# Performance work log

Measured on AMD Instinct MI355X. Metric: run time of the kernel, lower is better.

## Reference

```python
import jax, jax.numpy as jnp
import numpy as np

D = 256   # input_dim (also per-head dim)
H = 8     # num_heads
B = 32
S = 1024


def setup_inputs() -> dict:
    key = jax.random.key(0)
    ks = jax.random.split(key, 9)
    scale = 1.0 / np.sqrt(D)
    x = jax.random.normal(ks[0], (B, S, D), dtype=jnp.float32)
    Wk = jax.random.normal(ks[1], (D, D * H), dtype=jnp.float32) * scale
    bk = jnp.zeros((D * H,), dtype=jnp.float32)
    Wv = jax.random.normal(ks[2], (D, D * H), dtype=jnp.float32) * scale
    bv = jnp.zeros((D * H,), dtype=jnp.float32)
    query = jax.random.normal(ks[3], (H, D), dtype=jnp.float32)
    Wo = jax.random.normal(ks[4], (D * H, D), dtype=jnp.float32) / np.sqrt(D * H)
    bo = jnp.zeros((D,), dtype=jnp.float32)
    return {"x": x, "Wk": Wk, "bk": bk, "Wv": Wv, "bv": bv,
            "query": query, "Wo": Wo, "bo": bo}


def reference(x, Wk, bk, Wv, bv, query, Wo, bo):
    b, s, _ = x.shape
    # keys/values: [B, S, H, D]
    keys = (x @ Wk + bk).reshape(b, s, H, D)
    values = (x @ Wv + bv).reshape(b, s, H, D)
    # per-head single-query scores over sequence: [B, S, H]
    scores = jnp.einsum("bshd,hd->bsh", keys, query)
    attn = jax.nn.softmax(scores, axis=1)
    # attention-pooled values per head: [B, H, D] -> concat [B, H*D]
    pooled = jnp.einsum("bsh,bshd->bhd", attn, values).reshape(b, H * D)
    return pooled @ Wo + bo
```

## Files before the change

### kernel.cpp

```cpp
#include <hip/hip_runtime.h>

#define D 256
#define H 8
#define B 32
#define S 1024
#define SCH 16
#define SCS 64

#define OFF_QK     0
#define OFF_SB     2048
#define OFF_ML     2056
#define OFF_XWP    10248
#define OFF_POOLED 1058824

__global__ void __launch_bounds__(256) k_prep(
        const float* __restrict__ Wk, const float* __restrict__ bk,
        const float* __restrict__ query, const float* __restrict__ bo,
        const float* __restrict__ bv,
        float* __restrict__ qk, float* __restrict__ sb,
        float* __restrict__ out, float* __restrict__ pooled) {
    __shared__ float red[256];
    const int h  = blockIdx.x >> 5;
    const int kc = blockIdx.x & 31;
    const int t  = threadIdx.x;
    const int kl = t >> 5;
    const int dq = t & 31;
    const int k  = kc * 8 + kl;
    const int d0 = dq * 8;
    const float* wrow = Wk + (size_t)k * (D * H) + h * D + d0;
    const float* qrow = query + h * D + d0;
    const float4 w0 = *(const float4*)(wrow);
    const float4 w1 = *(const float4*)(wrow + 4);
    const float4 q0 = *(const float4*)(qrow);
    const float4 q1 = *(const float4*)(qrow + 4);
    float acc = w0.x * q0.x + w0.y * q0.y + w0.z * q0.z + w0.w * q0.w
              + w1.x * q1.x + w1.y * q1.y + w1.z * q1.z + w1.w * q1.w;
    #pragma unroll
    for (int msk = 1; msk < 32; msk <<= 1) acc += __shfl_xor(acc, msk);
    if (dq == 0) qk[h * D + k] = acc;
    if (kc == 0) {
        red[t] = bk[h * D + t] * query[h * D + t];
        __syncthreads();
        for (int st = 128; st > 0; st >>= 1) {
            if (t < st) red[t] += red[t + st];
            __syncthreads();
        }
        if (t == 0) sb[h] = red[0];
    }
    pooled[(size_t)kc * (D * H) + h * D + t] = bv[h * D + t];
    if (h == 0) out[(size_t)kc * D + t] = bo[t];
}

__global__ void __launch_bounds__(256) k_fused(
        const float* __restrict__ x, const float* __restrict__ qk,
        const float* __restrict__ sb, float* __restrict__ xwp,
        float2* __restrict__ mlbuf) {
    const int b  = blockIdx.x >> 4;
    const int c  = blockIdx.x & 15;
    const int s0 = c * SCS;
    const int t  = threadIdx.x;
    __shared__ float qkL[H * D];
    __shared__ float sbL[H];
    __shared__ float sc[SCS][H];
    {
        float4* q4 = (float4*)qkL;
        q4[t]       = ((const float4*)qk)[t];
        q4[t + 256] = ((const float4*)qk)[t + 256];
        if (t < H) sbL[t] = sb[t];
    }
    __syncthreads();

    {
        const int sl = t >> 2;
        const int dq = t & 3;
        const int d0 = dq * 64;
        const float* xrow = x + ((size_t)(b * S + s0 + sl)) * D + d0;
        float accA[H] = {};
        #pragma unroll
        for (int j0 = 0; j0 < 16; j0++) {
            const int j = (j0 + dq * 4) & 15;
            const float4 xv = *(const float4*)(xrow + j * 4);
            #pragma unroll
            for (int hh = 0; hh < H; hh++) {
                const float4 qv = *(const float4*)(&qkL[hh * D + d0 + j * 4]);
                accA[hh] += xv.x * qv.x + xv.y * qv.y + xv.z * qv.z + xv.w * qv.w;
            }
        }
        #pragma unroll
        for (int hh = 0; hh < H; hh++) {
            accA[hh] += __shfl_xor(accA[hh], 1);
            accA[hh] += __shfl_xor(accA[hh], 2);
        }
        if (dq == 0) {
            #pragma unroll
            for (int hh = 0; hh < H; hh++)
                sc[sl][hh] = accA[hh] + sbL[hh];
        }
    }
    __syncthreads();

    {
        const int hh = t >> 5;
        const int u  = t & 31;
        const float v0 = sc[u][hh], v1 = sc[u + 32][hh];
        float m = fmaxf(v0, v1);
        #pragma unroll
        for (int msk = 1; msk < 32; msk <<= 1) m = fmaxf(m, __shfl_xor(m, msk));
        const float e0 = __expf(v0 - m), e1 = __expf(v1 - m);
        float sum = e0 + e1;
        #pragma unroll
        for (int msk = 1; msk < 32; msk <<= 1) sum += __shfl_xor(sum, msk);
        sc[u][hh] = e0;
        sc[u + 32][hh] = e1;
        if (u == 0) mlbuf[((size_t)(b * SCH + c)) * H + hh] = make_float2(m, sum);
    }
    __syncthreads();

    {
        float acc2[H] = {};
        const float* xp = x + ((size_t)(b * S + s0)) * D + t;
        #pragma unroll 4
        for (int s = 0; s < SCS; s++) {
            const float xv = xp[(size_t)s * D];
            const float4 pa = *(const float4*)(&sc[s][0]);
            const float4 pb = *(const float4*)(&sc[s][4]);
            acc2[0] += pa.x * xv; acc2[1] += pa.y * xv;
            acc2[2] += pa.z * xv; acc2[3] += pa.w * xv;
            acc2[4] += pb.x * xv; acc2[5] += pb.y * xv;
            acc2[6] += pb.z * xv; acc2[7] += pb.w * xv;
        }
        #pragma unroll
        for (int hh = 0; hh < H; hh++)
            xwp[(((size_t)(b * SCH + c)) * H + hh) * D + t] = acc2[hh];
    }
}

__global__ void __launch_bounds__(256) k_pooled(
        const float* __restrict__ xwp, const float2* __restrict__ mlbuf,
        const float* __restrict__ Wv, float* __restrict__ pooled) {
    const int blk = blockIdx.x;
    const int bh  = blk >> 1;
    const int dh  = blk & 1;
    const int b = bh >> 3, h = bh & 7;
    const int j = threadIdx.x;
    __shared__ float xwL[D / 2];
    __shared__ float scaleL[SCH];
    __shared__ float2 mlL[SCH];
    if (j < SCH) mlL[j] = mlbuf[((size_t)(b * SCH + j)) * H + h];
    __syncthreads();
    if (j == 0) {
        float M = -1e30f;
        for (int cc = 0; cc < SCH; cc++) M = fmaxf(M, mlL[cc].x);
        float L = 0.f;
        for (int cc = 0; cc < SCH; cc++) L += mlL[cc].y * __expf(mlL[cc].x - M);
        const float invL = 1.f / L;
        for (int cc = 0; cc < SCH; cc++) scaleL[cc] = __expf(mlL[cc].x - M) * invL;
    }
    __syncthreads();
    if (j < D / 2) {
        const int d = dh * (D / 2) + j;
        float acc = 0.f;
        #pragma unroll
        for (int cc = 0; cc < SCH; cc++)
            acc += xwp[(((size_t)(b * SCH + cc)) * H + h) * D + d] * scaleL[cc];
        xwL[j] = acc;
    }
    __syncthreads();
    const float* wcol = Wv + (size_t)(dh * (D / 2)) * (D * H) + h * D + j;
    float a2 = 0.f;
    #pragma unroll 8
    for (int d = 0; d < D / 2; d++)
        a2 += xwL[d] * wcol[(size_t)d * (D * H)];
    atomicAdd(pooled + (size_t)b * (D * H) + h * D + j, a2);
}

__global__ void __launch_bounds__(256) k_out(
        const float* __restrict__ pooled, const float* __restrict__ Wo,
        float* __restrict__ out) {
    const int b  = blockIdx.x >> 4;
    const int kc = blockIdx.x & 15;
    const int j  = threadIdx.x;
    __shared__ float pL[128];
    if (j < 128) pL[j] = pooled[(size_t)b * (D * H) + kc * 128 + j];
    __syncthreads();
    const float* wp = Wo + (size_t)(kc * 128) * D + j;
    float acc = 0.f;
    #pragma unroll 8
    for (int cc = 0; cc < 128; cc++)
        acc += pL[cc] * wp[(size_t)cc * D];
    atomicAdd(out + (size_t)b * D + j, acc);
}

extern "C" void kernel_launch(void* const* d_in, const int* in_sizes, int n_in,
                              void* d_out, int out_size, void* d_ws, size_t ws_size,
                              hipStream_t stream) {
    const float* x     = (const float*)d_in[0];
    const float* Wk    = (const float*)d_in[1];
    const float* bk    = (const float*)d_in[2];
    const float* Wv    = (const float*)d_in[3];
    const float* bv    = (const float*)d_in[4];
    const float* query = (const float*)d_in[5];
    const float* Wo    = (const float*)d_in[6];
    const float* bo    = (const float*)d_in[7];
    float* out = (float*)d_out;
    float* ws  = (float*)d_ws;

    float*  qk     = ws + OFF_QK;
    float*  sb     = ws + OFF_SB;
    float2* mlbuf  = (float2*)(ws + OFF_ML);
    float*  xwp    = ws + OFF_XWP;
    float*  pooled = ws + OFF_POOLED;

    k_prep<<<dim3(H * 32), dim3(256), 0, stream>>>(Wk, bk, query, bo, bv, qk, sb, out, pooled);
    k_fused<<<dim3(B * SCH), dim3(256), 0, stream>>>(x, qk, sb, xwp, mlbuf);
    k_pooled<<<dim3(B * H * 2), dim3(256), 0, stream>>>(xwp, mlbuf, Wv, pooled);
    k_out<<<dim3(B * 16), dim3(256), 0, stream>>>(pooled, Wo, out);
}
```

Baseline: 115.2 us.

## Fuse four kernels into one persistent kernel with software grid barriers

Replaces the prep, fused-score, pooled and output kernels with a single 256-block, 512-thread kernel that separates the phases with atomic-counter grid barriers. A memset of the barrier counters is added to the launch. The pooled and output projections are merged within each block, which removes the pooled workspace round trip and its atomics. The goal is to cut the launch gaps between the four kernels. In exchange it relies on all 256 blocks being co-resident, and the barrier spin has a timeout that could silently break correctness.

```diff
diff --git a/kernel.cpp b/kernel.cpp
--- a/kernel.cpp
+++ b/kernel.cpp
@@ -7,188 +7,206 @@
 #define SCH 16
 #define SCS 64
 
-#define OFF_QK     0
-#define OFF_SB     2048
-#define OFF_ML     2056
-#define OFF_XWP    10248
-#define OFF_POOLED 1058824
-
-__global__ void __launch_bounds__(256) k_prep(
-        const float* __restrict__ Wk, const float* __restrict__ bk,
-        const float* __restrict__ query, const float* __restrict__ bo,
-        const float* __restrict__ bv,
-        float* __restrict__ qk, float* __restrict__ sb,
-        float* __restrict__ out, float* __restrict__ pooled) {
-    __shared__ float red[256];
-    const int h  = blockIdx.x >> 5;
-    const int kc = blockIdx.x & 31;
-    const int t  = threadIdx.x;
-    const int kl = t >> 5;
-    const int dq = t & 31;
-    const int k  = kc * 8 + kl;
-    const int d0 = dq * 8;
-    const float* wrow = Wk + (size_t)k * (D * H) + h * D + d0;
-    const float* qrow = query + h * D + d0;
-    const float4 w0 = *(const float4*)(wrow);
-    const float4 w1 = *(const float4*)(wrow + 4);
-    const float4 q0 = *(const float4*)(qrow);
-    const float4 q1 = *(const float4*)(qrow + 4);
-    float acc = w0.x * q0.x + w0.y * q0.y + w0.z * q0.z + w0.w * q0.w
-              + w1.x * q1.x + w1.y * q1.y + w1.z * q1.z + w1.w * q1.w;
-    #pragma unroll
-    for (int msk = 1; msk < 32; msk <<= 1) acc += __shfl_xor(acc, msk);
-    if (dq == 0) qk[h * D + k] = acc;
-    if (kc == 0) {
-        red[t] = bk[h * D + t] * query[h * D + t];
-        __syncthreads();
-        for (int st = 128; st > 0; st >>= 1) {
-            if (t < st) red[t] += red[t + st];
-            __syncthreads();
-        }
-        if (t == 0) sb[h] = red[0];
-    }
-    pooled[(size_t)kc * (D * H) + h * D + t] = bv[h * D + t];
-    if (h == 0) out[(size_t)kc * D + t] = bo[t];
+#define NBLK 256
+#define NTHR 512
+
+#define OFF_QK   0
+#define OFF_SB   2048
+#define OFF_ML   2056
+#define OFF_XWP  10248
+#define OFF_BAR  1058824
+
+__device__ __forceinline__ void grid_barrier(int* cnt, int* gen) {
+    __syncthreads();
+    if (threadIdx.x == 0) {
+        const int g = __hip_atomic_load(gen, __ATOMIC_RELAXED, __HIP_MEMORY_SCOPE_AGENT);
+        const int v = __hip_atomic_fetch_add(cnt, 1, __ATOMIC_ACQ_REL, __HIP_MEMORY_SCOPE_AGENT);
+        if (v == NBLK - 1) {
+            __hip_atomic_store(cnt, 0, __ATOMIC_RELAXED, __HIP_MEMORY_SCOPE_AGENT);
+            __hip_atomic_store(gen, g + 1, __ATOMIC_RELEASE, __HIP_MEMORY_SCOPE_AGENT);
+        } else {
+            int it = 0;
+            while (__hip_atomic_load(gen, __ATOMIC_ACQUIRE, __HIP_MEMORY_SCOPE_AGENT) == g) {
+                __builtin_amdgcn_s_sleep(2);
+                if (++it > 4000000) break;
+            }
+        }
+    }
+    __syncthreads();
 }
 
-__global__ void __launch_bounds__(256) k_fused(
-        const float* __restrict__ x, const float* __restrict__ qk,
-        const float* __restrict__ sb, float* __restrict__ xwp,
-        float2* __restrict__ mlbuf) {
-    const int b  = blockIdx.x >> 4;
-    const int c  = blockIdx.x & 15;
-    const int s0 = c * SCS;
-    const int t  = threadIdx.x;
-    __shared__ float qkL[H * D];
-    __shared__ float sbL[H];
-    __shared__ float sc[SCS][H];
+__global__ void __launch_bounds__(NTHR, 2) k_mega(
+        const float* __restrict__ x,  const float* __restrict__ Wk,
+        const float* __restrict__ bk, const float* __restrict__ Wv,
+        const float* __restrict__ bv, const float* __restrict__ query,
+        const float* __restrict__ Wo, const float* __restrict__ bo,
+        float* __restrict__ ws, float* __restrict__ out) {
+    __shared__ float  qkL[H * D];
+    __shared__ float  sbL[H];
+    __shared__ float  sc[2][SCS][H];
+    __shared__ float2 mlL[2][SCH];
+    __shared__ float  scaleL[2][SCH];
+    __shared__ float  xwL[2][D / 2];
+    __shared__ float  ppL[2][D];
+
+    float*  qk    = ws + OFF_QK;
+    float*  sb    = ws + OFF_SB;
+    float2* mlbuf = (float2*)(ws + OFF_ML);
+    float*  xwp   = ws + OFF_XWP;
+    int*    bar   = (int*)(ws + OFF_BAR);
+
+    const int bid = blockIdx.x;
+    const int t   = threadIdx.x;
+
     {
-        float4* q4 = (float4*)qkL;
-        q4[t]       = ((const float4*)qk)[t];
-        q4[t + 256] = ((const float4*)qk)[t + 256];
-        if (t < H) sbL[t] = sb[t];
-    }
-    __syncthreads();
+        const int w    = t >> 6;
+        const int lane = t & 63;
+        const int p    = bid * 8 + w;
+        const int h    = p >> 8, k = p & 255;
+        const float4 wv = *(const float4*)(Wk + (size_t)k * (D * H) + h * D + lane * 4);
+        const float4 qv = *(const float4*)(query + h * D + lane * 4);
+        float acc = wv.x * qv.x + wv.y * qv.y + wv.z * qv.z + wv.w * qv.w;
+        #pragma unroll
+        for (int m = 1; m < 64; m <<= 1) acc += __shfl_xor(acc, m);
+        if (lane == 0) qk[h * D + k] = acc;
+        if (bid < 8 && w == 0) {
+            const float4 bkv = *(const float4*)(bk + bid * D + lane * 4);
+            const float4 qv2 = *(const float4*)(query + bid * D + lane * 4);
+            float a2 = bkv.x * qv2.x + bkv.y * qv2.y + bkv.z * qv2.z + bkv.w * qv2.w;
+            #pragma unroll
+            for (int m = 1; m < 64; m <<= 1) a2 += __shfl_xor(a2, m);
+            if (lane == 0) sb[bid] = a2;
+        }
+        if (bid < 16) {
+            const int idx = bid * NTHR + t;
+            out[idx] = bo[idx & 255];
+        }
+    }
+    grid_barrier(bar, bar + 1);
 
     {
-        const int sl = t >> 2;
-        const int dq = t & 3;
-        const int d0 = dq * 64;
-        const float* xrow = x + ((size_t)(b * S + s0 + sl)) * D + d0;
-        float accA[H] = {};
-        #pragma unroll
-        for (int j0 = 0; j0 < 16; j0++) {
-            const int j = (j0 + dq * 4) & 15;
-            const float4 xv = *(const float4*)(xrow + j * 4);
+        const int half = t >> 8, tt = t & 255;
+        const int task = bid * 2 + half;
+        const int b = task >> 4, c = task & 15;
+        const int s0 = c * SCS;
+        {
+            ((float4*)qkL)[t] = ((const float4*)qk)[t];
+            if (t < H) sbL[t] = sb[t];
+        }
+        __syncthreads();
+
+        {
+            const int sl = tt >> 2;
+            const int dq = tt & 3;
+            const int d0 = dq * 64;
+            const float* xrow = x + ((size_t)(b * S + s0 + sl)) * D + d0;
+            float accA[H] = {};
+            #pragma unroll
+            for (int j0 = 0; j0 < 16; j0++) {
+                const int j = (j0 + dq * 4) & 15;
+                const float4 xv = *(const float4*)(xrow + j * 4);
+                #pragma unroll
+                for (int hh = 0; hh < H; hh++) {
+                    const float4 qv = *(const float4*)(&qkL[hh * D + d0 + j * 4]);
+                    accA[hh] += xv.x * qv.x + xv.y * qv.y + xv.z * qv.z + xv.w * qv.w;
+                }
+            }
             #pragma unroll
             for (int hh = 0; hh < H; hh++) {
-                const float4 qv = *(const float4*)(&qkL[hh * D + d0 + j * 4]);
-                accA[hh] += xv.x * qv.x + xv.y * qv.y + xv.z * qv.z + xv.w * qv.w;
-            }
-        }
-        #pragma unroll
-        for (int hh = 0; hh < H; hh++) {
-            accA[hh] += __shfl_xor(accA[hh], 1);
-            accA[hh] += __shfl_xor(accA[hh], 2);
-        }
-        if (dq == 0) {
+                accA[hh] += __shfl_xor(accA[hh], 1);
+                accA[hh] += __shfl_xor(accA[hh], 2);
+            }
+            if (dq == 0) {
+                #pragma unroll
+                for (int hh = 0; hh < H; hh++)
+                    sc[half][sl][hh] = accA[hh] + sbL[hh];
+            }
+        }
+        __syncthreads();
+
+        {
+            const int hh = tt >> 5;
+            const int u  = tt & 31;
+            const float v0 = sc[half][u][hh], v1 = sc[half][u + 32][hh];
+            float m = fmaxf(v0, v1);
+            #pragma unroll
+            for (int msk = 1; msk < 32; msk <<= 1) m = fmaxf(m, __shfl_xor(m, msk));
+            const float e0 = __expf(v0 - m), e1 = __expf(v1 - m);
+            float sum = e0 + e1;
+            #pragma unroll
+            for (int msk = 1; msk < 32; msk <<= 1) sum += __shfl_xor(sum, msk);
+            sc[half][u][hh] = e0;
+            sc[half][u + 32][hh] = e1;
+            if (u == 0) mlbuf[((size_t)(b * SCH + c)) * H + hh] = make_float2(m, sum);
+        }
+        __syncthreads();
+
+        {
+            float acc2[H] = {};
+            const float* xp = x + ((size_t)(b * S + s0)) * D + tt;
+            #pragma unroll 4
+            for (int s = 0; s < SCS; s++) {
+                const float xv = xp[(size_t)s * D];
+                const float4 pa = *(const float4*)(&sc[half][s][0]);
+                const float4 pb = *(const float4*)(&sc[half][s][4]);
+                acc2[0] += pa.x * xv; acc2[1] += pa.y * xv;
+                acc2[2] += pa.z * xv; acc2[3] += pa.w * xv;
+                acc2[4] += pb.x * xv; acc2[5] += pb.y * xv;
+                acc2[6] += pb.z * xv; acc2[7] += pb.w * xv;
+            }
             #pragma unroll
             for (int hh = 0; hh < H; hh++)
-                sc[sl][hh] = accA[hh] + sbL[hh];
-        }
-    }
-    __syncthreads();
+                xwp[(((size_t)(b * SCH + c)) * H + hh) * D + tt] = acc2[hh];
+        }
+    }
+    grid_barrier(bar, bar + 1);
 
     {
-        const int hh = t >> 5;
-        const int u  = t & 31;
-        const float v0 = sc[u][hh], v1 = sc[u + 32][hh];
-        float m = fmaxf(v0, v1);
-        #pragma unroll
-        for (int msk = 1; msk < 32; msk <<= 1) m = fmaxf(m, __shfl_xor(m, msk));
-        const float e0 = __expf(v0 - m), e1 = __expf(v1 - m);
-        float sum = e0 + e1;
-        #pragma unroll
-        for (int msk = 1; msk < 32; msk <<= 1) sum += __shfl_xor(sum, msk);
-        sc[u][hh] = e0;
-        sc[u + 32][hh] = e1;
-        if (u == 0) mlbuf[((size_t)(b * SCH + c)) * H + hh] = make_float2(m, sum);
-    }
-    __syncthreads();
-
-    {
-        float acc2[H] = {};
-        const float* xp = x + ((size_t)(b * S + s0)) * D + t;
-        #pragma unroll 4
-        for (int s = 0; s < SCS; s++) {
-            const float xv = xp[(size_t)s * D];
-            const float4 pa = *(const float4*)(&sc[s][0]);
-            const float4 pb = *(const float4*)(&sc[s][4]);
-            acc2[0] += pa.x * xv; acc2[1] += pa.y * xv;
-            acc2[2] += pa.z * xv; acc2[3] += pa.w * xv;
-            acc2[4] += pb.x * xv; acc2[5] += pb.y * xv;
-            acc2[6] += pb.z * xv; acc2[7] += pb.w * xv;
-        }
-        #pragma unroll
-        for (int hh = 0; hh < H; hh++)
-            xwp[(((size_t)(b * SCH + c)) * H + hh) * D + t] = acc2[hh];
-    }
-}
-
-__global__ void __launch_bounds__(256) k_pooled(
-        const float* __restrict__ xwp, const float2* __restrict__ mlbuf,
-        const float* __restrict__ Wv, float* __restrict__ pooled) {
-    const int blk = blockIdx.x;
-    const int bh  = blk >> 1;
-    const int dh  = blk & 1;
-    const int b = bh >> 3, h = bh & 7;
-    const int j = threadIdx.x;
-    __shared__ float xwL[D / 2];
-    __shared__ float scaleL[SCH];
-    __shared__ float2 mlL[SCH];
-    if (j < SCH) mlL[j] = mlbuf[((size_t)(b * SCH + j)) * H + h];
-    __syncthreads();
-    if (j == 0) {
-        float M = -1e30f;
-        for (int cc = 0; cc < SCH; cc++) M = fmaxf(M, mlL[cc].x);
-        float L = 0.f;
-        for (int cc = 0; cc < SCH; cc++) L += mlL[cc].y * __expf(mlL[cc].x - M);
-        const float invL = 1.f / L;
-        for (int cc = 0; cc < SCH; cc++) scaleL[cc] = __expf(mlL[cc].x - M) * invL;
-    }
-    __syncthreads();
-    if (j < D / 2) {
-        const int d = dh * (D / 2) + j;
-        float acc = 0.f;
-        #pragma unroll
-        for (int cc = 0; cc < SCH; cc++)
-            acc += xwp[(((size_t)(b * SCH + cc)) * H + h) * D + d] * scaleL[cc];
-        xwL[j] = acc;
-    }
-    __syncthreads();
-    const float* wcol = Wv + (size_t)(dh * (D / 2)) * (D * H) + h * D + j;
-    float a2 = 0.f;
-    #pragma unroll 8
-    for (int d = 0; d < D / 2; d++)
-        a2 += xwL[d] * wcol[(size_t)d * (D * H)];
-    atomicAdd(pooled + (size_t)b * (D * H) + h * D + j, a2);
-}
-
-__global__ void __launch_bounds__(256) k_out(
-        const float* __restrict__ pooled, const float* __restrict__ Wo,
-        float* __restrict__ out) {
-    const int b  = blockIdx.x >> 4;
-    const int kc = blockIdx.x & 15;
-    const int j  = threadIdx.x;
-    __shared__ float pL[128];
-    if (j < 128) pL[j] = pooled[(size_t)b * (D * H) + kc * 128 + j];
-    __syncthreads();
-    const float* wp = Wo + (size_t)(kc * 128) * D + j;
-    float acc = 0.f;
-    #pragma unroll 8
-    for (int cc = 0; cc < 128; cc++)
-        acc += pL[cc] * wp[(size_t)cc * D];
-    atomicAdd(out + (size_t)b * D + j, acc);
+        const int half = t >> 8, tt = t & 255;
+        const int dh = half;
+        const int b = bid >> 3, h = bid & 7;
+        if (tt < SCH) mlL[half][tt] = mlbuf[((size_t)(b * SCH + tt)) * H + h];
+        __syncthreads();
+        if (tt == 0) {
+            float M = -1e30f;
+            for (int cc = 0; cc < SCH; cc++) M = fmaxf(M, mlL[half][cc].x);
+            float L = 0.f;
+            for (int cc = 0; cc < SCH; cc++) L += mlL[half][cc].y * __expf(mlL[half][cc].x - M);
+            const float invL = 1.f / L;
+            for (int cc = 0; cc < SCH; cc++) scaleL[half][cc] = __expf(mlL[half][cc].x - M) * invL;
+        }
+        __syncthreads();
+        if (tt < D / 2) {
+            const int d = dh * (D / 2) + tt;
+            float acc = 0.f;
+            #pragma unroll
+            for (int cc = 0; cc < SCH; cc++)
+                acc += xwp[(((size_t)(b * SCH + cc)) * H + h) * D + d] * scaleL[half][cc];
+            xwL[half][tt] = acc;
+        }
+        __syncthreads();
+        {
+            const float* wcol = Wv + (size_t)(dh * (D / 2)) * (D * H) + h * D + tt;
+            float a2 = 0.f;
+            #pragma unroll 8
+            for (int d = 0; d < D / 2; d++)
+                a2 += xwL[half][d] * wcol[(size_t)d * (D * H)];
+            if (dh == 0) a2 += bv[h * D + tt];
+            ppL[half][tt] = a2;
+        }
+        __syncthreads();
+        if (half == 0) ppL[0][tt] += ppL[1][tt];
+        __syncthreads();
+        {
+            const int j0 = half * 128;
+            const float* wp = Wo + (size_t)(h * D + j0) * D + tt;
+            float o = 0.f;
+            #pragma unroll 8
+            for (int jj = 0; jj < 128; jj++)
+                o += ppL[0][j0 + jj] * wp[(size_t)jj * D];
+            atomicAdd(out + (size_t)b * D + tt, o);
+        }
+    }
 }
 
 extern "C" void kernel_launch(void* const* d_in, const int* in_sizes, int n_in,
@@ -205,14 +223,8 @@
     float* out = (float*)d_out;
     float* ws  = (float*)d_ws;
 
-    float*  qk     = ws + OFF_QK;
-    float*  sb     = ws + OFF_SB;
-    float2* mlbuf  = (float2*)(ws + OFF_ML);
-    float*  xwp    = ws + OFF_XWP;
-    float*  pooled = ws + OFF_POOLED;
-
-    k_prep<<<dim3(H * 32), dim3(256), 0, stream>>>(Wk, bk, query, bo, bv, qk, sb, out, pooled);
-    k_fused<<<dim3(B * SCH), dim3(256), 0, stream>>>(x, qk, sb, xwp, mlbuf);
-    k_pooled<<<dim3(B * H * 2), dim3(256), 0, stream>>>(xwp, mlbuf, Wv, pooled);
-    k_out<<<dim3(B * 16), dim3(256), 0, stream>>>(pooled, Wo, out);
+    hipMemsetAsync((char*)d_ws + (size_t)OFF_BAR * sizeof(float), 0,
+                   2 * sizeof(int), stream);
+    k_mega<<<dim3(NBLK), dim3(NTHR), 0, stream>>>(
+        x, Wk, bk, Wv, bv, query, Wo, bo, ws, out);
 }
```

New measurement: 171.5 us. +49.0%, slower.

## Split sequence into 64 chunks of 16 and parallelize chunk softmax merge

Applied to the files above, without the earlier changes.

Shrinks each sequence chunk in the fused score/softmax/x-weighting kernel from 64 to 16 rows, quadrupling the number of blocks to 2048 so more CUs are busy. The score dot-product is restructured so 16 threads share each row, and the per-chunk softmax uses 16-lane reductions. The chunk merge in the pooled kernel now uses wavefront shuffles instead of a single serial thread. The cost is a 4x larger partial buffer (xwp) that has to be written and then re-read when merging, and more chunks to combine per (b,h).

```diff
diff --git a/kernel.cpp b/kernel.cpp
--- a/kernel.cpp
+++ b/kernel.cpp
@@ -4,14 +4,14 @@
 #define H 8
 #define B 32
 #define S 1024
-#define SCH 16
-#define SCS 64
+#define SCH 64
+#define SCS 16
 
 #define OFF_QK     0
 #define OFF_SB     2048
 #define OFF_ML     2056
-#define OFF_XWP    10248
-#define OFF_POOLED 1058824
+#define OFF_XWP    34824
+#define OFF_POOLED 4229128
 
 __global__ void __launch_bounds__(256) k_prep(
         const float* __restrict__ Wk, const float* __restrict__ bk,
@@ -51,12 +51,12 @@
     if (h == 0) out[(size_t)kc * D + t] = bo[t];
 }
 
-__global__ void __launch_bounds__(256) k_fused(
+__global__ void __launch_bounds__(256, 6) k_fused(
         const float* __restrict__ x, const float* __restrict__ qk,
         const float* __restrict__ sb, float* __restrict__ xwp,
         float2* __restrict__ mlbuf) {
-    const int b  = blockIdx.x >> 4;
-    const int c  = blockIdx.x & 15;
+    const int b  = blockIdx.x >> 6;
+    const int c  = blockIdx.x & 63;
     const int s0 = c * SCS;
     const int t  = threadIdx.x;
     __shared__ float qkL[H * D];
@@ -71,25 +71,37 @@
     __syncthreads();
 
     {
-        const int sl = t >> 2;
-        const int dq = t & 3;
-        const int d0 = dq * 64;
+        const int sl = t >> 4;
+        const int dq = t & 15;
+        const int d0 = dq * 16;
         const float* xrow = x + ((size_t)(b * S + s0 + sl)) * D + d0;
+        const int o0 = ((dq    ) & 3) * 4;
+        const int o1 = ((dq + 1) & 3) * 4;
+        const int o2 = ((dq + 2) & 3) * 4;
+        const int o3 = ((dq + 3) & 3) * 4;
+        const float4 xa = *(const float4*)(xrow + o0);
+        const float4 xb = *(const float4*)(xrow + o1);
+        const float4 xc = *(const float4*)(xrow + o2);
+        const float4 xd = *(const float4*)(xrow + o3);
         float accA[H] = {};
         #pragma unroll
-        for (int j0 = 0; j0 < 16; j0++) {
-            const int j = (j0 + dq * 4) & 15;
-            const float4 xv = *(const float4*)(xrow + j * 4);
-            #pragma unroll
-            for (int hh = 0; hh < H; hh++) {
-                const float4 qv = *(const float4*)(&qkL[hh * D + d0 + j * 4]);
-                accA[hh] += xv.x * qv.x + xv.y * qv.y + xv.z * qv.z + xv.w * qv.w;
-            }
+        for (int hh = 0; hh < H; hh++) {
+            const float* qb = &qkL[hh * D + d0];
+            const float4 qa = *(const float4*)(qb + o0);
+            const float4 q1 = *(const float4*)(qb + o1);
+            const float4 q2 = *(const float4*)(qb + o2);
+            const float4 q3 = *(const float4*)(qb + o3);
+            accA[hh] = xa.x * qa.x + xa.y * qa.y + xa.z * qa.z + xa.w * qa.w
+                     + xb.x * q1.x + xb.y * q1.y + xb.z * q1.z + xb.w * q1.w
+                     + xc.x * q2.x + xc.y * q2.y + xc.z * q2.z + xc.w * q2.w
+                     + xd.x * q3.x + xd.y * q3.y + xd.z * q3.z + xd.w * q3.w;
         }
         #pragma unroll
         for (int hh = 0; hh < H; hh++) {
             accA[hh] += __shfl_xor(accA[hh], 1);
             accA[hh] += __shfl_xor(accA[hh], 2);
+            accA[hh] += __shfl_xor(accA[hh], 4);
+            accA[hh] += __shfl_xor(accA[hh], 8);
         }
         if (dq == 0) {
             #pragma unroll
@@ -99,19 +111,18 @@
     }
     __syncthreads();
 
-    {
-        const int hh = t >> 5;
-        const int u  = t & 31;
-        const float v0 = sc[u][hh], v1 = sc[u + 32][hh];
-        float m = fmaxf(v0, v1);
-        #pragma unroll
-        for (int msk = 1; msk < 32; msk <<= 1) m = fmaxf(m, __shfl_xor(m, msk));
-        const float e0 = __expf(v0 - m), e1 = __expf(v1 - m);
-        float sum = e0 + e1;
-        #pragma unroll
-        for (int msk = 1; msk < 32; msk <<= 1) sum += __shfl_xor(sum, msk);
-        sc[u][hh] = e0;
-        sc[u + 32][hh] = e1;
+    if (t < 128) {
+        const int hh = t >> 4;
+        const int u  = t & 15;
+        const float v = sc[u][hh];
+        float m = v;
+        #pragma unroll
+        for (int msk = 1; msk < 16; msk <<= 1) m = fmaxf(m, __shfl_xor(m, msk));
+        const float e = __expf(v - m);
+        float sum = e;
+        #pragma unroll
+        for (int msk = 1; msk < 16; msk <<= 1) sum += __shfl_xor(sum, msk);
+        sc[u][hh] = e;
         if (u == 0) mlbuf[((size_t)(b * SCH + c)) * H + hh] = make_float2(m, sum);
     }
     __syncthreads();
@@ -119,7 +130,7 @@
     {
         float acc2[H] = {};
         const float* xp = x + ((size_t)(b * S + s0)) * D + t;
-        #pragma unroll 4
+        #pragma unroll
         for (int s = 0; s < SCS; s++) {
             const float xv = xp[(size_t)s * D];
             const float4 pa = *(const float4*)(&sc[s][0]);
@@ -145,22 +156,22 @@
     const int j = threadIdx.x;
     __shared__ float xwL[D / 2];
     __shared__ float scaleL[SCH];
-    __shared__ float2 mlL[SCH];
-    if (j < SCH) mlL[j] = mlbuf[((size_t)(b * SCH + j)) * H + h];
-    __syncthreads();
-    if (j == 0) {
-        float M = -1e30f;
-        for (int cc = 0; cc < SCH; cc++) M = fmaxf(M, mlL[cc].x);
-        float L = 0.f;
-        for (int cc = 0; cc < SCH; cc++) L += mlL[cc].y * __expf(mlL[cc].x - M);
-        const float invL = 1.f / L;
-        for (int cc = 0; cc < SCH; cc++) scaleL[cc] = __expf(mlL[cc].x - M) * invL;
+    if (j < SCH) {
+        const float2 ml = mlbuf[((size_t)(b * SCH + j)) * H + h];
+        float M = ml.x;
+        #pragma unroll
+        for (int msk = 1; msk < 64; msk <<= 1) M = fmaxf(M, __shfl_xor(M, msk));
+        const float p = __expf(ml.x - M);
+        float L = ml.y * p;
+        #pragma unroll
+        for (int msk = 1; msk < 64; msk <<= 1) L += __shfl_xor(L, msk);
+        scaleL[j] = p / L;
     }
     __syncthreads();
     if (j < D / 2) {
         const int d = dh * (D / 2) + j;
         float acc = 0.f;
-        #pragma unroll
+        #pragma unroll 8
         for (int cc = 0; cc < SCH; cc++)
             acc += xwp[(((size_t)(b * SCH + cc)) * H + h) * D + d] * scaleL[cc];
         xwL[j] = acc;
```

Result: slower. 122.6 us (+6.5%).

## Fuse Wv and Wo projections into one kernel and double sequence chunks

Applied to the files above, without the earlier changes.

Merges the pooled-value projection and the output projection into a single kernel, which removes the pooled workspace buffer and one kernel launch. Each block computes a half-slice of pooled for one (b,h), adds bv, and atomically accumulates its partial Wo product into out. The sequence chunking changes from 16x64 to 32x32, which doubles the number of k_fused blocks, and the score kernel is restructured to preload x into registers. The xwp and ml workspace layouts are transposed so that reads in the combine kernel are contiguous. In exchange, xwp traffic doubles and there are more atomics on out.

```diff
diff --git a/kernel.cpp b/kernel.cpp
--- a/kernel.cpp
+++ b/kernel.cpp
@@ -4,21 +4,19 @@
 #define H 8
 #define B 32
 #define S 1024
-#define SCH 16
-#define SCS 64
-
-#define OFF_QK     0
-#define OFF_SB     2048
-#define OFF_ML     2056
-#define OFF_XWP    10248
-#define OFF_POOLED 1058824
+#define SCH 32
+#define SCS 32
+
+#define OFF_QK   0
+#define OFF_SB   2048
+#define OFF_ML   2056
+#define OFF_XWP  18440
 
 __global__ void __launch_bounds__(256) k_prep(
         const float* __restrict__ Wk, const float* __restrict__ bk,
         const float* __restrict__ query, const float* __restrict__ bo,
-        const float* __restrict__ bv,
         float* __restrict__ qk, float* __restrict__ sb,
-        float* __restrict__ out, float* __restrict__ pooled) {
+        float* __restrict__ out) {
     __shared__ float red[256];
     const int h  = blockIdx.x >> 5;
     const int kc = blockIdx.x & 31;
@@ -47,16 +45,15 @@
         }
         if (t == 0) sb[h] = red[0];
     }
-    pooled[(size_t)kc * (D * H) + h * D + t] = bv[h * D + t];
     if (h == 0) out[(size_t)kc * D + t] = bo[t];
 }
 
-__global__ void __launch_bounds__(256) k_fused(
+__global__ void __launch_bounds__(256, 4) k_fused(
         const float* __restrict__ x, const float* __restrict__ qk,
         const float* __restrict__ sb, float* __restrict__ xwp,
         float2* __restrict__ mlbuf) {
-    const int b  = blockIdx.x >> 4;
-    const int c  = blockIdx.x & 15;
+    const int b  = blockIdx.x >> 5;
+    const int c  = blockIdx.x & 31;
     const int s0 = c * SCS;
     const int t  = threadIdx.x;
     __shared__ float qkL[H * D];
@@ -71,25 +68,35 @@
     __syncthreads();
 
     {
-        const int sl = t >> 2;
-        const int dq = t & 3;
-        const int d0 = dq * 64;
+        const int sl = t >> 3;
+        const int dq = t & 7;
+        const int d0 = dq * 32;
         const float* xrow = x + ((size_t)(b * S + s0 + sl)) * D + d0;
-        float accA[H] = {};
-        #pragma unroll
-        for (int j0 = 0; j0 < 16; j0++) {
-            const int j = (j0 + dq * 4) & 15;
-            const float4 xv = *(const float4*)(xrow + j * 4);
+        float4 xr[8];
+        #pragma unroll
+        for (int j0 = 0; j0 < 8; j0++) {
+            const int je = (j0 + dq) & 7;
+            xr[j0] = *(const float4*)(xrow + je * 4);
+        }
+        float accA[H];
+        #pragma unroll
+        for (int hh = 0; hh < H; hh++) {
+            const float* qb = &qkL[hh * D + d0];
+            float a = 0.f;
             #pragma unroll
-            for (int hh = 0; hh < H; hh++) {
-                const float4 qv = *(const float4*)(&qkL[hh * D + d0 + j * 4]);
-                accA[hh] += xv.x * qv.x + xv.y * qv.y + xv.z * qv.z + xv.w * qv.w;
+            for (int j0 = 0; j0 < 8; j0++) {
+                const int je = (j0 + dq) & 7;
+                const float4 qv = *(const float4*)(qb + je * 4);
+                a += xr[j0].x * qv.x + xr[j0].y * qv.y
+                   + xr[j0].z * qv.z + xr[j0].w * qv.w;
             }
+            accA[hh] = a;
         }
         #pragma unroll
         for (int hh = 0; hh < H; hh++) {
             accA[hh] += __shfl_xor(accA[hh], 1);
             accA[hh] += __shfl_xor(accA[hh], 2);
+            accA[hh] += __shfl_xor(accA[hh], 4);
         }
         if (dq == 0) {
             #pragma unroll
@@ -102,24 +109,23 @@
     {
         const int hh = t >> 5;
         const int u  = t & 31;
-        const float v0 = sc[u][hh], v1 = sc[u + 32][hh];
-        float m = fmaxf(v0, v1);
+        const float v = sc[u][hh];
+        float m = v;
         #pragma unroll
         for (int msk = 1; msk < 32; msk <<= 1) m = fmaxf(m, __shfl_xor(m, msk));
-        const float e0 = __expf(v0 - m), e1 = __expf(v1 - m);
-        float sum = e0 + e1;
+        const float e = __expf(v - m);
+        float sum = e;
         #pragma unroll
         for (int msk = 1; msk < 32; msk <<= 1) sum += __shfl_xor(sum, msk);
-        sc[u][hh] = e0;
-        sc[u + 32][hh] = e1;
-        if (u == 0) mlbuf[((size_t)(b * SCH + c)) * H + hh] = make_float2(m, sum);
+        sc[u][hh] = e;
+        if (u == 0) mlbuf[((size_t)(b * H + hh)) * SCH + c] = make_float2(m, sum);
     }
     __syncthreads();
 
     {
         float acc2[H] = {};
         const float* xp = x + ((size_t)(b * S + s0)) * D + t;
-        #pragma unroll 4
+        #pragma unroll 8
         for (int s = 0; s < SCS; s++) {
             const float xv = xp[(size_t)s * D];
             const float4 pa = *(const float4*)(&sc[s][0]);
@@ -131,64 +137,66 @@
         }
         #pragma unroll
         for (int hh = 0; hh < H; hh++)
-            xwp[(((size_t)(b * SCH + c)) * H + hh) * D + t] = acc2[hh];
-    }
-}
-
-__global__ void __launch_bounds__(256) k_pooled(
+            xwp[(((size_t)(b * H + hh)) * SCH + c) * D + t] = acc2[hh];
+    }
+}
+
+__global__ void __launch_bounds__(256, 4) k_po(
         const float* __restrict__ xwp, const float2* __restrict__ mlbuf,
-        const float* __restrict__ Wv, float* __restrict__ pooled) {
+        const float* __restrict__ Wv, const float* __restrict__ bv,
+        const float* __restrict__ Wo, float* __restrict__ out) {
     const int blk = blockIdx.x;
+    const int dvh = blk & 1;
     const int bh  = blk >> 1;
-    const int dh  = blk & 1;
     const int b = bh >> 3, h = bh & 7;
-    const int j = threadIdx.x;
-    __shared__ float xwL[D / 2];
+    const int t = threadIdx.x;
     __shared__ float scaleL[SCH];
-    __shared__ float2 mlL[SCH];
-    if (j < SCH) mlL[j] = mlbuf[((size_t)(b * SCH + j)) * H + h];
-    __syncthreads();
-    if (j == 0) {
-        float M = -1e30f;
-        for (int cc = 0; cc < SCH; cc++) M = fmaxf(M, mlL[cc].x);
-        float L = 0.f;
-        for (int cc = 0; cc < SCH; cc++) L += mlL[cc].y * __expf(mlL[cc].x - M);
-        const float invL = 1.f / L;
-        for (int cc = 0; cc < SCH; cc++) scaleL[cc] = __expf(mlL[cc].x - M) * invL;
-    }
-    __syncthreads();
-    if (j < D / 2) {
-        const int d = dh * (D / 2) + j;
+    __shared__ float xwL[D];
+    __shared__ float pp[256];
+    __shared__ float pooledL[128];
+
+    if (t < SCH) {
+        const float2 ml = mlbuf[((size_t)(b * H + h)) * SCH + t];
+        float M = ml.x;
+        #pragma unroll
+        for (int msk = 1; msk < 32; msk <<= 1) M = fmaxf(M, __shfl_xor(M, msk));
+        const float p = __expf(ml.x - M);
+        float L = ml.y * p;
+        #pragma unroll
+        for (int msk = 1; msk < 32; msk <<= 1) L += __shfl_xor(L, msk);
+        scaleL[t] = p / L;
+    }
+    __syncthreads();
+    {
+        const float* xp = xwp + ((size_t)(b * H + h)) * SCH * D + t;
         float acc = 0.f;
-        #pragma unroll
+        #pragma unroll 8
         for (int cc = 0; cc < SCH; cc++)
-            acc += xwp[(((size_t)(b * SCH + cc)) * H + h) * D + d] * scaleL[cc];
-        xwL[j] = acc;
-    }
-    __syncthreads();
-    const float* wcol = Wv + (size_t)(dh * (D / 2)) * (D * H) + h * D + j;
-    float a2 = 0.f;
-    #pragma unroll 8
-    for (int d = 0; d < D / 2; d++)
-        a2 += xwL[d] * wcol[(size_t)d * (D * H)];
-    atomicAdd(pooled + (size_t)b * (D * H) + h * D + j, a2);
-}
-
-__global__ void __launch_bounds__(256) k_out(
-        const float* __restrict__ pooled, const float* __restrict__ Wo,
-        float* __restrict__ out) {
-    const int b  = blockIdx.x >> 4;
-    const int kc = blockIdx.x & 15;
-    const int j  = threadIdx.x;
-    __shared__ float pL[128];
-    if (j < 128) pL[j] = pooled[(size_t)b * (D * H) + kc * 128 + j];
-    __syncthreads();
-    const float* wp = Wo + (size_t)(kc * 128) * D + j;
-    float acc = 0.f;
-    #pragma unroll 8
-    for (int cc = 0; cc < 128; cc++)
-        acc += pL[cc] * wp[(size_t)cc * D];
-    atomicAdd(out + (size_t)b * D + j, acc);
+            acc += xp[(size_t)cc * D] * scaleL[cc];
+        xwL[t] = acc;
+    }
+    __syncthreads();
+    {
+        const int kseg = t >> 7;
+        const int dvl  = t & 127;
+        const float* wp = Wv + (size_t)(kseg * 128) * (D * H) + h * D + dvh * 128 + dvl;
+        float acc = 0.f;
+        #pragma unroll 8
+        for (int dd = 0; dd < 128; dd++)
+            acc += xwL[kseg * 128 + dd] * wp[(size_t)dd * (D * H)];
+        pp[t] = acc;
+    }
+    __syncthreads();
+    if (t < 128) pooledL[t] = pp[t] + pp[t + 128] + bv[h * D + dvh * 128 + t];
+    __syncthreads();
+    {
+        const float* wo = Wo + (size_t)(h * D + dvh * 128) * D + t;
+        float acc = 0.f;
+        #pragma unroll 8
+        for (int dv = 0; dv < 128; dv++)
+            acc += pooledL[dv] * wo[(size_t)dv * D];
+        atomicAdd(out + (size_t)b * D + t, acc);
+    }
 }
 
 extern "C" void kernel_launch(void* const* d_in, const int* in_sizes, int n_in,
@@ -205,14 +213,12 @@
     float* out = (float*)d_out;
     float* ws  = (float*)d_ws;
 
-    float*  qk     = ws + OFF_QK;
-    float*  sb     = ws + OFF_SB;
-    float2* mlbuf  = (float2*)(ws + OFF_ML);
-    float*  xwp    = ws + OFF_XWP;
-    float*  pooled = ws + OFF_POOLED;
-
-    k_prep<<<dim3(H * 32), dim3(256), 0, stream>>>(Wk, bk, query, bo, bv, qk, sb, out, pooled);
+    float*  qk    = ws + OFF_QK;
+    float*  sb    = ws + OFF_SB;
+    float2* mlbuf = (float2*)(ws + OFF_ML);
+    float*  xwp   = ws + OFF_XWP;
+
+    k_prep<<<dim3(H * 32), dim3(256), 0, stream>>>(Wk, bk, query, bo, qk, sb, out);
     k_fused<<<dim3(B * SCH), dim3(256), 0, stream>>>(x, qk, sb, xwp, mlbuf);
-    k_pooled<<<dim3(B * H * 2), dim3(256), 0, stream>>>(xwp, mlbuf, Wv, pooled);
-    k_out<<<dim3(B * 16), dim3(256), 0, stream>>>(pooled, Wo, out);
-}
+    k_po<<<dim3(B * H * 2), dim3(256), 0, stream>>>(xwp, mlbuf, Wv, bv, Wo, out);
+}
```

Result: slower. 118.5 us (+2.9%).
